# Kernel tuning notes

Measured on AMD Instinct MI355X. Metric: run time of the kernel, lower is better.

Reference implementation:

```python
import jax, jax.numpy as jnp
import numpy as np

NUM_EXPERT = 16
IN_FEAT = 1024
OUT_FEAT = 4096
N_TOKENS = 2048


def setup_inputs() -> dict:
    key = jax.random.key(0)
    k1, k2, k3 = jax.random.split(key, 3)
    inp = jax.random.normal(k1, (N_TOKENS, IN_FEAT), dtype=jnp.float32)
    gate = jax.random.randint(k2, (N_TOKENS,), 0, NUM_EXPERT, dtype=jnp.int32)
    # reset_parameters() fills each expert with nn.Linear weights:
    # kaiming-uniform, effectively U(-1/sqrt(in_feat), 1/sqrt(in_feat))
    bound = 1.0 / np.sqrt(IN_FEAT)
    weight = jax.random.uniform(
        k3, (NUM_EXPERT, OUT_FEAT, IN_FEAT), dtype=jnp.float32,
        minval=-bound, maxval=bound)
    return {"inp": inp, "gate": gate, "weight": weight}


def reference(inp, gate, weight):
    # Grouped GEMM: out[n] = weight[gate[n]] @ inp[n]
    # Expressed as dense one-hot dispatch -> per-expert GEMM -> combine,
    # which computes the identical math without materializing a per-token
    # [N, out, in] gathered weight tensor.
    onehot = jax.nn.one_hot(gate, NUM_EXPERT, dtype=inp.dtype)       # [N, E]
    dispatched = jnp.einsum('ne,nd->end', onehot, inp)               # [E, N, in]
    expert_out = jnp.einsum('end,eod->eno', dispatched, weight)      # [E, N, out]
    out = jnp.einsum('ne,eno->no', onehot, expert_out)               # [N, out]
    return out
```

## Files before the change

### kernel.cpp

```cpp
#include <hip/hip_runtime.h>
#include <hip/hip_bf16.h>

#define NEXP 16
#define KDIM 1024
#define ODIM 4096
#define NTOK 2048

#define BM   256
#define BN   128
#define KC   32
#define NPH  (KDIM / KC)
#define NBLK (NEXP * (ODIM / BN))

typedef __attribute__((ext_vector_type(8))) short short8;
typedef __attribute__((ext_vector_type(4))) float f32x4;

typedef __attribute__((address_space(3))) unsigned lds_uint;
typedef const __attribute__((address_space(1))) unsigned glob_uint;

__device__ __forceinline__ void gload16(const void* g, void* l) {
    __builtin_amdgcn_global_load_lds((glob_uint*)g, (lds_uint*)l, 16, 0, 0);
}

__device__ __forceinline__ unsigned short f2bf(float f) {
    __hip_bfloat16 h = __float2bfloat16(f);
    return __builtin_bit_cast(unsigned short, h);
}

__device__ __forceinline__ short8 pack8(float4 a, float4 b) {
    short8 r;
    r[0] = (short)f2bf(a.x); r[1] = (short)f2bf(a.y);
    r[2] = (short)f2bf(a.z); r[3] = (short)f2bf(a.w);
    r[4] = (short)f2bf(b.x); r[5] = (short)f2bf(b.y);
    r[6] = (short)f2bf(b.z); r[7] = (short)f2bf(b.w);
    return r;
}

#define SFENCE() __builtin_amdgcn_sched_barrier(0)
#define WAITVM(N) do { SFENCE(); \
        asm volatile("s_waitcnt vmcnt(" #N ")" ::: "memory"); SFENCE(); } while (0)
#define WAITLG() do { SFENCE(); \
        asm volatile("s_waitcnt lgkmcnt(0)" ::: "memory"); SFENCE(); } while (0)

__global__ __launch_bounds__(256) void moe_sort(const int* __restrict__ gate,
                                                int* __restrict__ perm,
                                                int* __restrict__ offs) {
    __shared__ int lgate[NTOK];
    __shared__ int hist[256][NEXP + 1];
    __shared__ int base[NEXP];
    const int t = threadIdx.x;
    for (int i = t; i < NTOK; i += 256) lgate[i] = gate[i];
    #pragma unroll
    for (int e = 0; e < NEXP; ++e) hist[t][e] = 0;
    __syncthreads();
    const int TPT = NTOK / 256;
    for (int j = 0; j < TPT; ++j) hist[t][lgate[t * TPT + j]]++;
    __syncthreads();
    if (t < NEXP) {
        int s = 0;
        for (int i = 0; i < 256; ++i) { int v = hist[i][t]; hist[i][t] = s; s += v; }
        base[t] = s;
    }
    __syncthreads();
    if (t == 0) {
        int s = 0;
        for (int e = 0; e < NEXP; ++e) { int v = base[e]; base[e] = s; offs[e] = s; s += v; }
        offs[NEXP] = s;
    }
    __syncthreads();
    #pragma unroll
    for (int e = 0; e < NEXP; ++e) hist[t][e] += base[e];
    for (int j = 0; j < TPT; ++j) {
        int tok = t * TPT + j;
        int e = lgate[tok];
        int pos = hist[t][e]++;
        perm[pos] = tok;
    }
}

__global__ __launch_bounds__(256) void moe_cvt(const float* __restrict__ inp,
                                               const int* __restrict__ perm,
                                               unsigned short* __restrict__ A2T2) {
    const int o   = blockIdx.x;
    const int pos = blockIdx.y * 256 + threadIdx.x;
    const int tok = perm[pos];
    const float4* s = (const float4*)(inp + (size_t)tok * KDIM + o * 8);
    float4 v0 = s[0], v1 = s[1];
    *(short8*)(A2T2 + ((size_t)o * NTOK + pos) * 8) = pack8(v0, v1);
}

template <bool PRE>
__global__ __launch_bounds__(512, 4) void moe_gemm(
    const float* __restrict__ inp,
    const unsigned short* __restrict__ A2T2,
    const float* __restrict__ weight,
    const int* __restrict__ perm,
    const int* __restrict__ offs,
    float* __restrict__ out)
{
    const int bid = blockIdx.x;
    const int v   = (bid & 7) * (NBLK / 8) + (bid >> 3);
    const int e   = v >> 5;
    const int oc  = (v & 31) * BN;

    const int beg = offs[e], end = offs[e + 1];
    const int nall = end - beg;
    if (nall <= 0) return;

    __shared__ float Bs[2][BN][KC];
    __shared__ short As[2][4][BM][8];

    const int t    = threadIdx.x;
    const int lane = t & 63;
    const int w    = t >> 6;
    const int wm   = w >> 2;
    const int wn   = w & 3;
    const int frow = lane & 15;
    const int fks  = lane >> 4;

    const int brow = t >> 3;
    const int hs   = (t & 7) ^ ((t >> 3) & 7);
    const float* bsrc0 = weight + ((size_t)e * ODIM + oc + brow) * KDIM + hs * 4;
    const float* bsrc1 = bsrc0 + (size_t)64 * KDIM;

#define ISSUE_B(buf, kc) {                                                    \
        gload16(bsrc0 + (kc), (char*)&Bs[buf][0][0] + t * 16);                \
        gload16(bsrc1 + (kc), (char*)&Bs[buf][0][0] + 8192 + t * 16);         \
    }
#define ISSUE_A(buf, p) {                                                     \
        gload16(asrc0 + (size_t)(p) * (4 * NTOK * 8),                         \
                (char*)&As[buf][0][0][0] + t * 16);                           \
        gload16(asrc1 + (size_t)(p) * (4 * NTOK * 8),                         \
                (char*)&As[buf][0][0][0] + 8192 + t * 16);                    \
    }
#define NLOAD_A(p) {                                                          \
        A0a = *(const float4*)(afsrc + (p) * KC);                             \
        A0b = *(const float4*)(afsrc + (p) * KC + 4);                         \
        A1a = *(const float4*)(afsrc + (p) * KC + 16);                        \
        A1b = *(const float4*)(afsrc + (p) * KC + 20);                        \
    }
#define NWRITE_A(buf) {                                                       \
        *(short8*)((char*)&As[buf][0][0][0] + t * 16)        = pack8(A0a, A0b); \
        *(short8*)((char*)&As[buf][0][0][0] + 8192 + t * 16) = pack8(A1a, A1b); \
    }
#define STEP(buf) {                                                           \
        short8 bfr0, bfr1;                                                    \
        {                                                                     \
            int rB = wn * 32 + frow;                                          \
            int x  = rB & 7;                                                  \
            float4 lo = *(const float4*)((const char*)&Bs[buf][0][0]          \
                         + rB * 128 + (((2 * fks)     ^ x) * 16));            \
            float4 hi = *(const float4*)((const char*)&Bs[buf][0][0]          \
                         + rB * 128 + (((2 * fks + 1) ^ x) * 16));            \
            bfr0 = pack8(lo, hi);                                             \
            rB += 16;                                                         \
            lo = *(const float4*)((const char*)&Bs[buf][0][0]                 \
                         + rB * 128 + (((2 * fks)     ^ x) * 16));            \
            hi = *(const float4*)((const char*)&Bs[buf][0][0]                 \
                         + rB * 128 + (((2 * fks + 1) ^ x) * 16));            \
            bfr1 = pack8(lo, hi);                                             \
        }                                                                     \
        _Pragma("unroll")                                                     \
        for (int m = 0; m < 8; ++m) {                                         \
            if (m * 16 < mmax) {                                              \
                int row = wm * 128 + m * 16 + frow;                           \
                short8 af = *(const short8*)((const char*)&As[buf][0][0][0]   \
                             + fks * 4096 + row * 16);                        \
                acc[m][0] = __builtin_amdgcn_mfma_f32_16x16x32_bf16(af, bfr0, acc[m][0], 0, 0, 0); \
                acc[m][1] = __builtin_amdgcn_mfma_f32_16x16x32_bf16(af, bfr1, acc[m][1], 0, 0, 0); \
            }                                                                 \
        }                                                                     \
    }

    for (int base = 0; base < nall; base += BM) {
        const int rows = (nall - base < BM) ? (nall - base) : BM;
        const int c0   = beg + base;
        const int mmax = rows - wm * 128;

        int rcl = t & 255; if (rcl > rows - 1) rcl = rows - 1;
        const unsigned short* asrc0 = 0;
        const unsigned short* asrc1 = 0;
        const float* afsrc = 0;
        if (PRE) {
            const int g0 = t >> 8;
            asrc0 = A2T2 + ((size_t)g0       * NTOK + (c0 + rcl)) * 8;
            asrc1 = A2T2 + ((size_t)(g0 + 2) * NTOK + (c0 + rcl)) * 8;
        } else {
            afsrc = inp + (size_t)perm[c0 + rcl] * KDIM + (t >> 8) * 8;
        }

        f32x4 acc[8][2];
        #pragma unroll
        for (int m = 0; m < 8; ++m) {
            acc[m][0] = (f32x4){0.f, 0.f, 0.f, 0.f};
            acc[m][1] = (f32x4){0.f, 0.f, 0.f, 0.f};
        }
        float4 A0a, A0b, A1a, A1b;

        WAITLG();
        __builtin_amdgcn_s_barrier();

        if (PRE) {
            ISSUE_B(0, 0);  ISSUE_A(0, 0);
            ISSUE_B(1, KC); ISSUE_A(1, 1);
            WAITVM(4);
            __builtin_amdgcn_s_barrier();
            for (int p = 0; p < NPH; ++p) {
                const int cur = p & 1;
                STEP(cur);
                if (p + 1 < NPH) {
                    WAITLG();
                    __builtin_amdgcn_s_barrier();
                    if (p + 2 < NPH) {
                        ISSUE_B(cur, (p + 2) * KC);
                        ISSUE_A(cur, p + 2);
                        WAITVM(4);
                    } else {
                        WAITVM(0);
                    }
                    __builtin_amdgcn_s_barrier();
                }
            }
        } else {
            NLOAD_A(0); ISSUE_B(0, 0);  NWRITE_A(0);
            NLOAD_A(1); ISSUE_B(1, KC); NWRITE_A(1);
            WAITVM(0); WAITLG();
            __builtin_amdgcn_s_barrier();
            for (int p = 0; p < NPH; ++p) {
                const int cur = p & 1;
                if (p + 2 < NPH) NLOAD_A(p + 2);
                STEP(cur);
                if (p + 1 < NPH) {
                    WAITLG();
                    __builtin_amdgcn_s_barrier();
                    if (p + 2 < NPH) { ISSUE_B(cur, (p + 2) * KC); NWRITE_A(cur); }
                    WAITVM(0); WAITLG();
                    __builtin_amdgcn_s_barrier();
                }
            }
        }

        const int col0 = oc + wn * 32 + frow;
        #pragma unroll
        for (int m = 0; m < 8; ++m) {
            #pragma unroll
            for (int reg = 0; reg < 4; ++reg) {
                int r = wm * 128 + m * 16 + fks * 4 + reg;
                if (r < rows) {
                    int tok = perm[c0 + r];
                    float* orow = out + (size_t)tok * ODIM + col0;
                    orow[0]  = acc[m][0][reg];
                    orow[16] = acc[m][1][reg];
                }
            }
        }
    }
#undef ISSUE_B
#undef ISSUE_A
#undef NLOAD_A
#undef NWRITE_A
#undef STEP
}

extern "C" void kernel_launch(void* const* d_in, const int* in_sizes, int n_in,
                              void* d_out, int out_size, void* d_ws, size_t ws_size,
                              hipStream_t stream) {
    const float* inp    = (const float*)d_in[0];
    const int*   gate   = (const int*)d_in[1];
    const float* weight = (const float*)d_in[2];
    float*       out    = (float*)d_out;

    int* perm = (int*)d_ws;
    int* offs = perm + NTOK;
    unsigned short* A2T2 = (unsigned short*)((char*)d_ws + 16384);
    const size_t need = 16384 + (size_t)NTOK * KDIM * 2;
    const bool pre = (ws_size >= need);

    moe_sort<<<1, 256, 0, stream>>>(gate, perm, offs);
    if (pre) {
        dim3 cg(KDIM / 8, NTOK / 256);
        moe_cvt<<<cg, 256, 0, stream>>>(inp, perm, A2T2);
        moe_gemm<true><<<NBLK, 512, 0, stream>>>(inp, A2T2, weight, perm, offs, out);
    } else {
        moe_gemm<false><<<NBLK, 512, 0, stream>>>(inp, A2T2, weight, perm, offs, out);
    }
}
```

Measured before the change: 106.7 us.

## Load A fragments directly from global into registers, drop A LDS staging

Removes the shared-memory double buffer for the activation (A) tile and has each wave read its MFMA A fragments straight from the pre-converted bf16 buffer, or from fp32 input in the fallback path. This cuts LDS capacity use and LDS traffic, which could allow more resident blocks, and simplifies the pipeline to stage only the weights. In exchange, the A global loads are no longer prefetched ahead of use, so their latency sits on the critical path inside the MFMA loop. The same A rows are also fetched redundantly by each of the four column waves. The workspace size requirement is also padded, presumably so the last reads past the token range stay inside the allocation.

```diff
diff --git a/kernel.cpp b/kernel.cpp
--- a/kernel.cpp
+++ b/kernel.cpp
@@ -108,7 +108,6 @@
     if (nall <= 0) return;
 
     __shared__ float Bs[2][BN][KC];
-    __shared__ short As[2][4][BM][8];
 
     const int t    = threadIdx.x;
     const int lane = t & 63;
@@ -127,66 +126,22 @@
         gload16(bsrc0 + (kc), (char*)&Bs[buf][0][0] + t * 16);                \
         gload16(bsrc1 + (kc), (char*)&Bs[buf][0][0] + 8192 + t * 16);         \
     }
-#define ISSUE_A(buf, p) {                                                     \
-        gload16(asrc0 + (size_t)(p) * (4 * NTOK * 8),                         \
-                (char*)&As[buf][0][0][0] + t * 16);                           \
-        gload16(asrc1 + (size_t)(p) * (4 * NTOK * 8),                         \
-                (char*)&As[buf][0][0][0] + 8192 + t * 16);                    \
-    }
-#define NLOAD_A(p) {                                                          \
-        A0a = *(const float4*)(afsrc + (p) * KC);                             \
-        A0b = *(const float4*)(afsrc + (p) * KC + 4);                         \
-        A1a = *(const float4*)(afsrc + (p) * KC + 16);                        \
-        A1b = *(const float4*)(afsrc + (p) * KC + 20);                        \
-    }
-#define NWRITE_A(buf) {                                                       \
-        *(short8*)((char*)&As[buf][0][0][0] + t * 16)        = pack8(A0a, A0b); \
-        *(short8*)((char*)&As[buf][0][0][0] + 8192 + t * 16) = pack8(A1a, A1b); \
-    }
-#define STEP(buf) {                                                           \
-        short8 bfr0, bfr1;                                                    \
-        {                                                                     \
-            int rB = wn * 32 + frow;                                          \
-            int x  = rB & 7;                                                  \
-            float4 lo = *(const float4*)((const char*)&Bs[buf][0][0]          \
-                         + rB * 128 + (((2 * fks)     ^ x) * 16));            \
-            float4 hi = *(const float4*)((const char*)&Bs[buf][0][0]          \
-                         + rB * 128 + (((2 * fks + 1) ^ x) * 16));            \
-            bfr0 = pack8(lo, hi);                                             \
-            rB += 16;                                                         \
-            lo = *(const float4*)((const char*)&Bs[buf][0][0]                 \
-                         + rB * 128 + (((2 * fks)     ^ x) * 16));            \
-            hi = *(const float4*)((const char*)&Bs[buf][0][0]                 \
-                         + rB * 128 + (((2 * fks + 1) ^ x) * 16));            \
-            bfr1 = pack8(lo, hi);                                             \
-        }                                                                     \
-        _Pragma("unroll")                                                     \
-        for (int m = 0; m < 8; ++m) {                                         \
-            if (m * 16 < mmax) {                                              \
-                int row = wm * 128 + m * 16 + frow;                           \
-                short8 af = *(const short8*)((const char*)&As[buf][0][0][0]   \
-                             + fks * 4096 + row * 16);                        \
-                acc[m][0] = __builtin_amdgcn_mfma_f32_16x16x32_bf16(af, bfr0, acc[m][0], 0, 0, 0); \
-                acc[m][1] = __builtin_amdgcn_mfma_f32_16x16x32_bf16(af, bfr1, acc[m][1], 0, 0, 0); \
-            }                                                                 \
-        }                                                                     \
-    }
 
     for (int base = 0; base < nall; base += BM) {
         const int rows = (nall - base < BM) ? (nall - base) : BM;
         const int c0   = beg + base;
         const int mmax = rows - wm * 128;
 
-        int rcl = t & 255; if (rcl > rows - 1) rcl = rows - 1;
-        const unsigned short* asrc0 = 0;
-        const unsigned short* asrc1 = 0;
-        const float* afsrc = 0;
+        const unsigned short* abase = 0;
+        int tok8[8];
         if (PRE) {
-            const int g0 = t >> 8;
-            asrc0 = A2T2 + ((size_t)g0       * NTOK + (c0 + rcl)) * 8;
-            asrc1 = A2T2 + ((size_t)(g0 + 2) * NTOK + (c0 + rcl)) * 8;
+            abase = A2T2 + ((size_t)fks * NTOK + (c0 + wm * 128 + frow)) * 8;
         } else {
-            afsrc = inp + (size_t)perm[c0 + rcl] * KDIM + (t >> 8) * 8;
+            #pragma unroll
+            for (int m = 0; m < 8; ++m) {
+                int r = wm * 128 + m * 16 + frow; if (r > rows - 1) r = rows - 1;
+                tok8[m] = perm[c0 + r];
+            }
         }
 
         f32x4 acc[8][2];
@@ -195,49 +150,58 @@
             acc[m][0] = (f32x4){0.f, 0.f, 0.f, 0.f};
             acc[m][1] = (f32x4){0.f, 0.f, 0.f, 0.f};
         }
-        float4 A0a, A0b, A1a, A1b;
 
         WAITLG();
         __builtin_amdgcn_s_barrier();
-
-        if (PRE) {
-            ISSUE_B(0, 0);  ISSUE_A(0, 0);
-            ISSUE_B(1, KC); ISSUE_A(1, 1);
-            WAITVM(4);
+        ISSUE_B(0, 0);
+        ISSUE_B(1, KC);
+        WAITVM(2);
+        __builtin_amdgcn_s_barrier();
+
+        for (int p = 0; p < NPH; ++p) {
+            const int cur = p & 1;
+            {
+                int rB = wn * 32 + frow;
+                const int x = rB & 7;
+                float4 lo = *(const float4*)((const char*)&Bs[cur][0][0]
+                             + rB * 128 + (((2 * fks)     ^ x) * 16));
+                float4 hi = *(const float4*)((const char*)&Bs[cur][0][0]
+                             + rB * 128 + (((2 * fks + 1) ^ x) * 16));
+                short8 bfr0 = pack8(lo, hi);
+                rB += 16;
+                lo = *(const float4*)((const char*)&Bs[cur][0][0]
+                             + rB * 128 + (((2 * fks)     ^ x) * 16));
+                hi = *(const float4*)((const char*)&Bs[cur][0][0]
+                             + rB * 128 + (((2 * fks + 1) ^ x) * 16));
+                short8 bfr1 = pack8(lo, hi);
+                #pragma unroll
+                for (int m = 0; m < 8; ++m) {
+                    if (m * 16 < mmax) {
+                        short8 af;
+                        if (PRE) {
+                            af = *(const short8*)(abase + m * 128);
+                        } else {
+                            const float* fsrc = inp + (size_t)tok8[m] * KDIM
+                                                + (p * 4 + fks) * 8;
+                            af = pack8(*(const float4*)(fsrc),
+                                       *(const float4*)(fsrc + 4));
+                        }
+                        acc[m][0] = __builtin_amdgcn_mfma_f32_16x16x32_bf16(af, bfr0, acc[m][0], 0, 0, 0);
+                        acc[m][1] = __builtin_amdgcn_mfma_f32_16x16x32_bf16(af, bfr1, acc[m][1], 0, 0, 0);
+                    }
+                }
+            }
+            if (PRE) abase += (size_t)4 * NTOK * 8;
+
+            WAITLG();
             __builtin_amdgcn_s_barrier();
-            for (int p = 0; p < NPH; ++p) {
-                const int cur = p & 1;
-                STEP(cur);
-                if (p + 1 < NPH) {
-                    WAITLG();
-                    __builtin_amdgcn_s_barrier();
-                    if (p + 2 < NPH) {
-                        ISSUE_B(cur, (p + 2) * KC);
-                        ISSUE_A(cur, p + 2);
-                        WAITVM(4);
-                    } else {
-                        WAITVM(0);
-                    }
-                    __builtin_amdgcn_s_barrier();
-                }
-            }
-        } else {
-            NLOAD_A(0); ISSUE_B(0, 0);  NWRITE_A(0);
-            NLOAD_A(1); ISSUE_B(1, KC); NWRITE_A(1);
-            WAITVM(0); WAITLG();
-            __builtin_amdgcn_s_barrier();
-            for (int p = 0; p < NPH; ++p) {
-                const int cur = p & 1;
-                if (p + 2 < NPH) NLOAD_A(p + 2);
-                STEP(cur);
-                if (p + 1 < NPH) {
-                    WAITLG();
-                    __builtin_amdgcn_s_barrier();
-                    if (p + 2 < NPH) { ISSUE_B(cur, (p + 2) * KC); NWRITE_A(cur); }
-                    WAITVM(0); WAITLG();
-                    __builtin_amdgcn_s_barrier();
-                }
-            }
+            if (p + 2 < NPH) {
+                ISSUE_B(cur, (p + 2) * KC);
+                WAITVM(2);
+            } else {
+                WAITVM(0);
+            }
+            if (p + 1 < NPH) __builtin_amdgcn_s_barrier();
         }
 
         const int col0 = oc + wn * 32 + frow;
@@ -256,10 +220,6 @@
         }
     }
 #undef ISSUE_B
-#undef ISSUE_A
-#undef NLOAD_A
-#undef NWRITE_A
-#undef STEP
 }
 
 extern "C" void kernel_launch(void* const* d_in, const int* in_sizes, int n_in,
@@ -273,7 +233,7 @@
     int* perm = (int*)d_ws;
     int* offs = perm + NTOK;
     unsigned short* A2T2 = (unsigned short*)((char*)d_ws + 16384);
-    const size_t need = 16384 + (size_t)NTOK * KDIM * 2;
+    const size_t need = 16384 + (size_t)NTOK * KDIM * 2 + 65536;
     const bool pre = (ws_size >= need);
 
     moe_sort<<<1, 256, 0, stream>>>(gate, perm, offs);
```

Result: slower. 136.5 us (+27.9%).
